# Optimization experiments

Hardware: AMD Instinct MI355X
Metric: run time of the kernel (lower is better)

## Reference

```python
import jax, jax.numpy as jnp
import numpy as np

EPS = 1e-5  # torch LayerNorm default eps

def _mish(x):
    return x * jnp.tanh(jax.nn.softplus(x))

def _ln(x, g, b):
    mu = jnp.mean(x, axis=-1, keepdims=True)
    var = jnp.mean(jnp.square(x - mu), axis=-1, keepdims=True)
    return (x - mu) * jax.lax.rsqrt(var + EPS) * g + b

def setup_inputs() -> dict:
    key = jax.random.key(0)
    ks = jax.random.split(key, 10)
    B, D, O1, O2, O3 = 65536, 784, 512, 264, 128
    def lin(k, fan_in, shape):
        bound = 1.0 / np.sqrt(fan_in)
        return jax.random.uniform(k, shape, jnp.float32, -bound, bound)
    return {
        "x":  jax.random.uniform(ks[0], (B, D), jnp.float32),
        "W1": lin(ks[1], D,  (O1, D)),   # enFC1, bias=False
        "g1": jnp.ones((O1,), jnp.float32), "b1": jnp.zeros((O1,), jnp.float32),
        "W2": lin(ks[2], O1, (O2, O1)),  # enFC2, bias=False
        "g2": jnp.ones((O2,), jnp.float32), "b2": jnp.zeros((O2,), jnp.float32),
        "W3": lin(ks[3], O2, (O3, O2)),  # enFC3 with bias
        "b3": lin(ks[4], O2, (O3,)),
        "gh": jnp.ones((O3,), jnp.float32), "bh": jnp.zeros((O3,), jnp.float32),
        "D1": lin(ks[5], O3, (O2, O3)),  # deFC1, bias=False
        "g3": jnp.ones((O2,), jnp.float32), "b3n": jnp.zeros((O2,), jnp.float32),
        "D2": lin(ks[6], O2, (O1, O2)),  # deFC2, bias=False
        "g4": jnp.ones((O1,), jnp.float32), "b4": jnp.zeros((O1,), jnp.float32),
        "D3": lin(ks[7], O1, (D, O1)),   # deFC3 with bias
        "bo": lin(ks[8], O1, (D,)),
    }

def reference(x, W1, g1, b1, W2, g2, b2, W3, b3, gh, bh,
              D1, g3, b3n, D2, g4, b4, D3, bo):
    h = _mish(_ln(x @ W1.T, g1, b1))
    h = _mish(_ln(h @ W2.T, g2, b2))
    x_latent = _mish(_ln(h @ W3.T + b3, gh, bh))
    h = _mish(_ln(x_latent @ D1.T, g3, b3n))
    h = _mish(_ln(h @ D2.T, g4, b4))
    out = jax.nn.sigmoid(h @ D3.T + bo)
    return out, jnp.sum(jnp.abs(x_latent))
```

## Files before the change

### kernel.cpp

```cpp
#include <hip/hip_runtime.h>


typedef short bf16x8 __attribute__((ext_vector_type(8)));
typedef float f32x4  __attribute__((ext_vector_type(4)));

#define B_ROWS 65536
#define EPS_LN 1e-5f

static __device__ __forceinline__ unsigned short f2bf(float f) {
    union { float f; unsigned u; } v; v.f = f;
    unsigned r = v.u + 0x7FFFu + ((v.u >> 16) & 1u);
    return (unsigned short)(r >> 16);
}

static __device__ __forceinline__ float mish_f(float x) {
    if (x > 15.f) return x;
    float u = __expf(x);
    float p = __fmaf_rn(u, u, 2.f * u);
    return x * (p / (p + 2.f));
}

static __device__ __forceinline__ void glds16(const void* g, void* l) {
    typedef __attribute__((address_space(3))) unsigned lds_u32;
    typedef __attribute__((address_space(1))) const unsigned glb_u32;
    lds_u32* lp = (lds_u32*)l;
    unsigned lofs = __builtin_amdgcn_readfirstlane((unsigned)(unsigned long long)lp);
    lp = (lds_u32*)(unsigned long long)lofs;
    __builtin_amdgcn_global_load_lds((glb_u32*)g, lp, 16, 0, 0);
}

struct CvtArgs {
    const float* src[6];
    unsigned short* dst[6];
    int O[6], K[6], KP[6];
    int base[7];
};

__global__ void wpad_kernel(CvtArgs a) {
    int b = blockIdx.x;
    int seg = 0;
    while (b >= a.base[seg + 1]) ++seg;
    int r = b - a.base[seg];
    int O = a.O[seg], K = a.K[seg], KP = a.KP[seg];
    const float* s = a.src[seg];
    unsigned short* d = a.dst[seg];
    for (int c = threadIdx.x; c < KP; c += 256) {
        unsigned short v = 0;
        if (r < O && c < K) v = f2bf(s[(size_t)r * K + c]);
        d[(size_t)r * KP + c] = v;
    }
}

template<int KP, int ASTR, int KREAL, int OP, int OREAL, int OSTRIDE, int NKT,
         bool SRCF32, bool HASBIAS, bool ABS, bool LN>
__global__ __launch_bounds__(1024, 4)
void layer3(const void* __restrict__ Asrc,
            const unsigned short* __restrict__ Wp,
            const float* __restrict__ gam,
            const float* __restrict__ bet,
            const float* __restrict__ bias,
            void* __restrict__ Aout,
            float* __restrict__ partials,
            int cbase)
{
    constexpr int NT     = OP / 128;
    constexpr int NCH_W  = OP / 16;
    constexpr int ABYTES = 128 * 64;
    constexpr int WBYTES = OP * 64;

    __shared__ __align__(16) char smem[2 * ABYTES + 2 * WBYTES];

    const int tid  = threadIdx.x;
    const int wave = tid >> 6, lane = tid & 63;
    const int wr = wave >> 3, wc = wave & 7;
    const int lg = lane >> 4, lc = lane & 15;
    const int row0 = blockIdx.x * 128;

    size_t goW[2];
    int    loW[2];
#pragma unroll
    for (int i = 0; i < 2; ++i) {
        int j = wave + 16 * i;
        if (j < NCH_W) {
            int q = j * 64 + lane;
            int r = q >> 2;
            int sg = (q & 3) ^ ((r >> 1) & 3);
            goW[i] = ((size_t)(cbase + r) * KP + sg * 8) * 2;
            loW[i] = 2 * ABYTES + j * 1024;
        } else { goW[i] = 0; loW[i] = 0; }
    }
    size_t goA = 0; int loA = 0;
    if constexpr (!SRCF32) {
        if (wave < 8) {
            int q = wave * 64 + lane;
            int r = q >> 2;
            int sg = (q & 3) ^ ((r >> 1) & 3);
            goA = ((size_t)(row0 + r) * ASTR + sg * 8) * 2;
            loA = wave * 1024;
        }
    }

    const char* Wg = (const char*)Wp;
    const char* Ag = (const char*)Asrc;

    float4 rA0 = make_float4(0,0,0,0), rA1 = make_float4(0,0,0,0);
    const int ar = tid >> 2, as = tid & 3;
    const float* axp = (const float*)Asrc + (size_t)(row0 + ar) * ASTR + as * 8;
    const int aswz = ar * 64 + ((as ^ ((ar >> 1) & 3)) << 4);

    auto loadA1 = [&](int t) {
        int c0 = t * 32 + as * 8;
        rA0 = (c0     < KREAL) ? *(const float4*)(axp + t * 32)     : make_float4(0,0,0,0);
        rA1 = (c0 + 4 < KREAL) ? *(const float4*)(axp + t * 32 + 4) : make_float4(0,0,0,0);
    };
    auto pubA = [&](int bsel) {
        union { unsigned short us[8]; uint4 v; } u;
        u.us[0] = f2bf(rA0.x); u.us[1] = f2bf(rA0.y);
        u.us[2] = f2bf(rA0.z); u.us[3] = f2bf(rA0.w);
        u.us[4] = f2bf(rA1.x); u.us[5] = f2bf(rA1.y);
        u.us[6] = f2bf(rA1.z); u.us[7] = f2bf(rA1.w);
        *(uint4*)(smem + bsel * ABYTES + aswz) = u.v;
    };
    auto stageW = [&](int t, int bsel) {
#pragma unroll
        for (int i = 0; i < 2; ++i)
            if (wave + 16 * i < NCH_W)
                glds16(Wg + goW[i] + (size_t)t * 64, smem + loW[i] + bsel * WBYTES);
        if constexpr (!SRCF32) {
            if (wave < 8)
                glds16(Ag + goA + (size_t)t * 64, smem + loA + bsel * ABYTES);
        }
    };

    stageW(0, 0);
    if constexpr (SRCF32) {
        if (tid < 512) { loadA1(0); pubA(0); if (NKT > 1) loadA1(1); }
    }
    __syncthreads();

    f32x4 acc[4][NT];
#pragma unroll
    for (int a = 0; a < 4; ++a)
#pragma unroll
        for (int c = 0; c < NT; ++c) acc[a][c] = (f32x4){0.f, 0.f, 0.f, 0.f};

    const int fswz = ((lg ^ ((lc >> 1) & 3)) << 4);

    for (int t = 0; t < NKT; ++t) {
        const int bsel = t & 1;
        if (t + 1 < NKT) stageW(t + 1, bsel ^ 1);

        const char* Ab = smem + bsel * ABYTES + (wr * 64 + lc) * 64 + fswz;
        const char* Bb = smem + 2 * ABYTES + bsel * WBYTES + (wc * NT * 16 + lc) * 64 + fswz;
        bf16x8 afr[4], bfr[NT];
#pragma unroll
        for (int a = 0; a < 4; ++a) afr[a] = *(const bf16x8*)(Ab + a * 1024);
#pragma unroll
        for (int c = 0; c < NT; ++c) bfr[c] = *(const bf16x8*)(Bb + c * 1024);

        if constexpr (SRCF32) {
            if (tid < 512) {
                if (t + 1 < NKT) pubA(bsel ^ 1);
                if (t + 2 < NKT) loadA1(t + 2);
            }
        }
        __builtin_amdgcn_sched_barrier(0);
#pragma unroll
        for (int c = 0; c < NT; ++c)
#pragma unroll
            for (int a = 0; a < 4; ++a)
                acc[a][c] = __builtin_amdgcn_mfma_f32_16x16x32_bf16(afr[a], bfr[c], acc[a][c], 0, 0, 0);
        __syncthreads();
    }

    if constexpr (LN) {
        if constexpr (HASBIAS) {
#pragma unroll
            for (int c = 0; c < NT; ++c) {
                int col = wc * NT * 16 + c * 16 + lc;
                float bv = (col < OREAL) ? bias[col] : 0.f;
#pragma unroll
                for (int a = 0; a < 4; ++a)
#pragma unroll
                    for (int r = 0; r < 4; ++r) acc[a][c][r] += bv;
            }
        }
        float ps1[4][4], ps2[4][4];
#pragma unroll
        for (int a = 0; a < 4; ++a)
#pragma unroll
            for (int r = 0; r < 4; ++r) { ps1[a][r] = 0.f; ps2[a][r] = 0.f; }
#pragma unroll
        for (int a = 0; a < 4; ++a)
#pragma unroll
            for (int c = 0; c < NT; ++c)
#pragma unroll
                for (int r = 0; r < 4; ++r) {
                    float v = acc[a][c][r];
                    ps1[a][r] += v;
                    ps2[a][r] = __fmaf_rn(v, v, ps2[a][r]);
                }
#pragma unroll
        for (int m = 1; m < 16; m <<= 1)
#pragma unroll
            for (int a = 0; a < 4; ++a)
#pragma unroll
                for (int r = 0; r < 4; ++r) {
                    ps1[a][r] += __shfl_xor(ps1[a][r], m);
                    ps2[a][r] += __shfl_xor(ps2[a][r], m);
                }

        float* lnP  = (float*)smem;
        float* lnMR = (float*)smem + 2048;
        float* wsumP= (float*)smem + 2304;

        if (lc == 0) {
#pragma unroll
            for (int a = 0; a < 4; ++a)
#pragma unroll
                for (int r = 0; r < 4; ++r) {
                    int row = wr * 64 + a * 16 + lg * 4 + r;
                    lnP[row * 8 + wc]        = ps1[a][r];
                    lnP[1024 + row * 8 + wc] = ps2[a][r];
                }
        }
        __syncthreads();
        if (tid < 128) {
            float s1 = 0.f, s2 = 0.f;
#pragma unroll
            for (int w = 0; w < 8; ++w) { s1 += lnP[tid * 8 + w]; s2 += lnP[1024 + tid * 8 + w]; }
            float mu = s1 * (1.f / OREAL);
            float var = fmaxf(s2 * (1.f / OREAL) - mu * mu, 0.f);
            lnMR[tid]       = mu;
            lnMR[128 + tid] = rsqrtf(var + EPS_LN);
        }
        __syncthreads();

        float gcol[NT], bcol[NT];
#pragma unroll
        for (int c = 0; c < NT; ++c) {
            int col = wc * NT * 16 + c * 16 + lc;
            gcol[c] = (col < OREAL) ? gam[col] : 0.f;
            bcol[c] = (col < OREAL) ? bet[col] : 0.f;
        }

        float asum = 0.f;
        unsigned short* outp = (unsigned short*)Aout;
#pragma unroll
        for (int a = 0; a < 4; ++a)
#pragma unroll
            for (int r = 0; r < 4; ++r) {
                int rl = wr * 64 + a * 16 + lg * 4 + r;
                float mu = lnMR[rl], rs = lnMR[128 + rl];
                size_t rowoff = (size_t)(row0 + rl) * OSTRIDE;
#pragma unroll
                for (int c = 0; c < NT; ++c) {
                    int col = wc * NT * 16 + c * 16 + lc;
                    if (col < OSTRIDE) {
                        unsigned short outv = 0;
                        if (col < OREAL) {
                            float v = (acc[a][c][r] - mu) * rs * gcol[c] + bcol[c];
                            float mz = mish_f(v);
                            if (ABS) asum += fabsf(mz);
                            outv = f2bf(mz);
                        }
                        outp[rowoff + col] = outv;
                    }
                }
            }

        if constexpr (ABS) {
#pragma unroll
            for (int m = 1; m < 64; m <<= 1) asum += __shfl_xor(asum, m);
            if (lane == 0) wsumP[wave] = asum;
            __syncthreads();
            if (tid == 0) {
                float s = 0.f;
                for (int w = 0; w < 16; ++w) s += wsumP[w];
                partials[blockIdx.x] = s;
            }
        }
    } else {
        float* outp = (float*)Aout;
#pragma unroll
        for (int c = 0; c < NT; ++c) {
            int col = cbase + wc * NT * 16 + c * 16 + lc;
            bool ok = col < OREAL;
            float bv = ok ? bias[col] : 0.f;
#pragma unroll
            for (int a = 0; a < 4; ++a)
#pragma unroll
                for (int r = 0; r < 4; ++r) {
                    if (ok) {
                        int rl = wr * 64 + a * 16 + lg * 4 + r;
                        float v = acc[a][c][r] + bv;
                        outp[(size_t)(row0 + rl) * OSTRIDE + col] = 1.f / (1.f + __expf(-v));
                    }
                }
        }
    }
}

__global__ void reduce_abs(const float* __restrict__ partials, float* __restrict__ out) {
    __shared__ float sm[256];
    float s = 0.f;
    for (int i = threadIdx.x; i < 512; i += 256) s += partials[i];
    sm[threadIdx.x] = s;
    __syncthreads();
    for (int step = 128; step > 0; step >>= 1) {
        if (threadIdx.x < step) sm[threadIdx.x] += sm[threadIdx.x + step];
        __syncthreads();
    }
    if (threadIdx.x == 0) out[0] = sm[0];
}

extern "C" void kernel_launch(void* const* d_in, const int* in_sizes, int n_in,
                              void* d_out, int out_size, void* d_ws, size_t ws_size,
                              hipStream_t stream)
{
    const float* x   = (const float*)d_in[0];
    const float* W1  = (const float*)d_in[1];
    const float* g1  = (const float*)d_in[2];
    const float* b1  = (const float*)d_in[3];
    const float* W2  = (const float*)d_in[4];
    const float* g2  = (const float*)d_in[5];
    const float* b2  = (const float*)d_in[6];
    const float* W3  = (const float*)d_in[7];
    const float* b3  = (const float*)d_in[8];
    const float* gh  = (const float*)d_in[9];
    const float* bh  = (const float*)d_in[10];
    const float* D1  = (const float*)d_in[11];
    const float* g3  = (const float*)d_in[12];
    const float* b3n = (const float*)d_in[13];
    const float* D2  = (const float*)d_in[14];
    const float* g4  = (const float*)d_in[15];
    const float* b4  = (const float*)d_in[16];
    const float* D3  = (const float*)d_in[17];
    const float* bo  = (const float*)d_in[18];

    char* ws = (char*)d_ws;
    size_t off = 0;
    auto alloc = [&](size_t bytes) -> char* {
        char* p = ws + off;
        off += (bytes + 255) & ~(size_t)255;
        return p;
    };
    unsigned short* W1p = (unsigned short*)alloc((size_t)512 * 800 * 2);
    unsigned short* W2p = (unsigned short*)alloc((size_t)384 * 512 * 2);
    unsigned short* W3p = (unsigned short*)alloc((size_t)128 * 288 * 2);
    unsigned short* D1p = (unsigned short*)alloc((size_t)384 * 128 * 2);
    unsigned short* D2p = (unsigned short*)alloc((size_t)512 * 288 * 2);
    unsigned short* D3p = (unsigned short*)alloc((size_t)896 * 512 * 2);
    unsigned short* actP = (unsigned short*)alloc((size_t)B_ROWS * 512 * 2);
    unsigned short* actQ = (unsigned short*)alloc((size_t)B_ROWS * 288 * 2);
    unsigned short* actL = (unsigned short*)alloc((size_t)B_ROWS * 128 * 2);
    float* partials = (float*)alloc(512 * 4);

    CvtArgs ca;
    ca.src[0] = W1; ca.dst[0] = W1p; ca.O[0] = 512; ca.K[0] = 784; ca.KP[0] = 800;
    ca.src[1] = W2; ca.dst[1] = W2p; ca.O[1] = 264; ca.K[1] = 512; ca.KP[1] = 512;
    ca.src[2] = W3; ca.dst[2] = W3p; ca.O[2] = 128; ca.K[2] = 264; ca.KP[2] = 288;
    ca.src[3] = D1; ca.dst[3] = D1p; ca.O[3] = 264; ca.K[3] = 128; ca.KP[3] = 128;
    ca.src[4] = D2; ca.dst[4] = D2p; ca.O[4] = 512; ca.K[4] = 264; ca.KP[4] = 288;
    ca.src[5] = D3; ca.dst[5] = D3p; ca.O[5] = 784; ca.K[5] = 512; ca.KP[5] = 512;
    ca.base[0] = 0;    ca.base[1] = 512;  ca.base[2] = 896;
    ca.base[3] = 1024; ca.base[4] = 1408; ca.base[5] = 1920; ca.base[6] = 2816;
    wpad_kernel<<<2816, 256, 0, stream>>>(ca);

    const int NB = B_ROWS / 128;

    layer3<800, 784, 784, 512, 512, 512, 25, true,  false, false, true>
        <<<NB, 1024, 0, stream>>>(x, W1p, g1, b1, nullptr, actP, nullptr, 0);
    layer3<512, 512, 512, 384, 264, 288, 16, false, false, false, true>
        <<<NB, 1024, 0, stream>>>(actP, W2p, g2, b2, nullptr, actQ, nullptr, 0);
    layer3<288, 288, 288, 128, 128, 128, 9,  false, true,  true,  true>
        <<<NB, 1024, 0, stream>>>(actQ, W3p, gh, bh, b3, actL, partials, 0);
    layer3<128, 128, 128, 384, 264, 288, 4,  false, false, false, true>
        <<<NB, 1024, 0, stream>>>(actL, D1p, g3, b3n, nullptr, actQ, nullptr, 0);
    layer3<288, 288, 288, 512, 512, 512, 9,  false, false, false, true>
        <<<NB, 1024, 0, stream>>>(actQ, D2p, g4, b4, nullptr, actP, nullptr, 0);
    layer3<512, 512, 512, 512, 784, 784, 16, false, true,  false, false>
        <<<NB, 1024, 0, stream>>>(actP, D3p, nullptr, nullptr, bo, d_out, nullptr, 0);
    layer3<512, 512, 512, 384, 784, 784, 16, false, true,  false, false>
        <<<NB, 1024, 0, stream>>>(actP, D3p, nullptr, nullptr, bo, d_out, nullptr, 512);

    reduce_abs<<<1, 256, 0, stream>>>(partials, (float*)d_out + (size_t)B_ROWS * 784);
}
```

Baseline: 479.5 us.

## Triple-buffer K-loop staging with explicit vmcnt waits and raw barriers

Converts the GEMM K-loop from double to triple buffering in LDS, prefetching two tiles ahead instead of one. Weight and activation chunks are unified into one staging table. Full __syncthreads is replaced by per-wave s_waitcnt vmcnt counts plus a raw s_barrier, so waves only wait for the oldest outstanding tile. This aims to hide global-to-LDS latency better, at the cost of more LDS per block (possible occupancy loss) and fragile hand-counted waitcnt logic.

```diff
diff --git a/kernel.cpp b/kernel.cpp
--- a/kernel.cpp
+++ b/kernel.cpp
@@ -27,6 +27,24 @@
     unsigned lofs = __builtin_amdgcn_readfirstlane((unsigned)(unsigned long long)lp);
     lp = (lds_u32*)(unsigned long long)lofs;
     __builtin_amdgcn_global_load_lds((glb_u32*)g, lp, 16, 0, 0);
+}
+
+template<int N> __device__ __forceinline__ void vwait() {
+    if constexpr      (N <= 0) asm volatile("s_waitcnt vmcnt(0)" ::: "memory");
+    else if constexpr (N == 1) asm volatile("s_waitcnt vmcnt(1)" ::: "memory");
+    else if constexpr (N == 2) asm volatile("s_waitcnt vmcnt(2)" ::: "memory");
+    else if constexpr (N == 3) asm volatile("s_waitcnt vmcnt(3)" ::: "memory");
+    else if constexpr (N == 4) asm volatile("s_waitcnt vmcnt(4)" ::: "memory");
+    else if constexpr (N == 5) asm volatile("s_waitcnt vmcnt(5)" ::: "memory");
+    else if constexpr (N == 6) asm volatile("s_waitcnt vmcnt(6)" ::: "memory");
+    else if constexpr (N == 8) asm volatile("s_waitcnt vmcnt(8)" ::: "memory");
+    else                       asm volatile("s_waitcnt vmcnt(63)" ::: "memory");
+}
+
+static __device__ __forceinline__ void barrier_raw() {
+    asm volatile("" ::: "memory");
+    __builtin_amdgcn_s_barrier();
+    asm volatile("" ::: "memory");
 }
 
 struct CvtArgs {
@@ -54,7 +72,7 @@
 template<int KP, int ASTR, int KREAL, int OP, int OREAL, int OSTRIDE, int NKT,
          bool SRCF32, bool HASBIAS, bool ABS, bool LN>
 __global__ __launch_bounds__(1024, 4)
-void layer3(const void* __restrict__ Asrc,
+void layer4(const void* __restrict__ Asrc,
             const unsigned short* __restrict__ Wp,
             const float* __restrict__ gam,
             const float* __restrict__ bet,
@@ -63,12 +81,17 @@
             float* __restrict__ partials,
             int cbase)
 {
-    constexpr int NT     = OP / 128;
-    constexpr int NCH_W  = OP / 16;
-    constexpr int ABYTES = 128 * 64;
-    constexpr int WBYTES = OP * 64;
-
-    __shared__ __align__(16) char smem[2 * ABYTES + 2 * WBYTES];
+    constexpr int NT      = OP / 128;
+    constexpr int NCH_W   = OP / 16;
+    constexpr int NCH_TOT = NCH_W + (SRCF32 ? 0 : 8);
+    constexpr int MAXC    = (NCH_TOT + 15) / 16;
+    constexpr int ABYTES  = 128 * 64;
+    constexpr int WBYTES  = OP * 64;
+    constexpr int WBASE   = 3 * ABYTES;
+    constexpr int LVL     = (NCH_TOT - 1 - 0) / 16 + 1;
+    constexpr int LVH     = (NCH_TOT - 1 - 8) / 16 + 1;
+
+    __shared__ __align__(16) char smem[WBASE + 3 * WBYTES];
 
     const int tid  = threadIdx.x;
     const int wave = tid >> 6, lane = tid & 63;
@@ -76,67 +99,63 @@
     const int lg = lane >> 4, lc = lane & 15;
     const int row0 = blockIdx.x * 128;
 
-    size_t goW[2];
-    int    loW[2];
-#pragma unroll
-    for (int i = 0; i < 2; ++i) {
-        int j = wave + 16 * i;
-        if (j < NCH_W) {
-            int q = j * 64 + lane;
-            int r = q >> 2;
-            int sg = (q & 3) ^ ((r >> 1) & 3);
-            goW[i] = ((size_t)(cbase + r) * KP + sg * 8) * 2;
-            loW[i] = 2 * ABYTES + j * 1024;
-        } else { goW[i] = 0; loW[i] = 0; }
-    }
-    size_t goA = 0; int loA = 0;
-    if constexpr (!SRCF32) {
-        if (wave < 8) {
-            int q = wave * 64 + lane;
-            int r = q >> 2;
-            int sg = (q & 3) ^ ((r >> 1) & 3);
-            goA = ((size_t)(row0 + r) * ASTR + sg * 8) * 2;
-            loA = wave * 1024;
-        }
-    }
-
-    const char* Wg = (const char*)Wp;
-    const char* Ag = (const char*)Asrc;
-
-    float4 rA0 = make_float4(0,0,0,0), rA1 = make_float4(0,0,0,0);
+    const char* gp[MAXC];
+    int lo[MAXC], lstr[MAXC];
+#pragma unroll
+    for (int i = 0; i < MAXC; ++i) {
+        int c = wave + 16 * i;
+        gp[i] = nullptr; lo[i] = 0; lstr[i] = 0;
+        if (c < NCH_W) {
+            int row = c * 16 + (lane >> 2);
+            int sg = (lane & 3) ^ ((row >> 1) & 3);
+            gp[i] = (const char*)Wp + ((size_t)(cbase + row) * KP + sg * 8) * 2;
+            lo[i] = WBASE + c * 1024; lstr[i] = WBYTES;
+        } else if (c < NCH_TOT) {
+            int ca = c - NCH_W;
+            int row = ca * 16 + (lane >> 2);
+            int sg = (lane & 3) ^ ((row >> 1) & 3);
+            gp[i] = (const char*)Asrc + ((size_t)(row0 + row) * ASTR + sg * 8) * 2;
+            lo[i] = ca * 1024; lstr[i] = ABYTES;
+        }
+    }
+    auto stage = [&](int t, int b) {
+#pragma unroll
+        for (int i = 0; i < MAXC; ++i) {
+            int c = wave + 16 * i;
+            if (c < NCH_TOT)
+                glds16(gp[i] + (size_t)t * 64, smem + lo[i] + b * lstr[i]);
+        }
+    };
+
     const int ar = tid >> 2, as = tid & 3;
     const float* axp = (const float*)Asrc + (size_t)(row0 + ar) * ASTR + as * 8;
     const int aswz = ar * 64 + ((as ^ ((ar >> 1) & 3)) << 4);
+    float4 rA0 = make_float4(0,0,0,0), rA1 = make_float4(0,0,0,0);
 
     auto loadA1 = [&](int t) {
         int c0 = t * 32 + as * 8;
         rA0 = (c0     < KREAL) ? *(const float4*)(axp + t * 32)     : make_float4(0,0,0,0);
         rA1 = (c0 + 4 < KREAL) ? *(const float4*)(axp + t * 32 + 4) : make_float4(0,0,0,0);
     };
-    auto pubA = [&](int bsel) {
+    auto pubA = [&](int b) {
         union { unsigned short us[8]; uint4 v; } u;
         u.us[0] = f2bf(rA0.x); u.us[1] = f2bf(rA0.y);
         u.us[2] = f2bf(rA0.z); u.us[3] = f2bf(rA0.w);
         u.us[4] = f2bf(rA1.x); u.us[5] = f2bf(rA1.y);
         u.us[6] = f2bf(rA1.z); u.us[7] = f2bf(rA1.w);
-        *(uint4*)(smem + bsel * ABYTES + aswz) = u.v;
+        *(uint4*)(smem + b * ABYTES + aswz) = u.v;
     };
-    auto stageW = [&](int t, int bsel) {
-#pragma unroll
-        for (int i = 0; i < 2; ++i)
-            if (wave + 16 * i < NCH_W)
-                glds16(Wg + goW[i] + (size_t)t * 64, smem + loW[i] + bsel * WBYTES);
-        if constexpr (!SRCF32) {
-            if (wave < 8)
-                glds16(Ag + goA + (size_t)t * 64, smem + loA + bsel * ABYTES);
-        }
-    };
-
-    stageW(0, 0);
+
+    stage(0, 0);
+    if constexpr (SRCF32) { if (tid < 512) loadA1(0); }
+    stage(1, 1);
     if constexpr (SRCF32) {
-        if (tid < 512) { loadA1(0); pubA(0); if (NKT > 1) loadA1(1); }
-    }
-    __syncthreads();
+        if (tid < 512) {
+            pubA(0);
+            loadA1(1);
+            asm volatile("s_waitcnt lgkmcnt(0)" ::: "memory");
+        }
+    }
 
     f32x4 acc[4][NT];
 #pragma unroll
@@ -146,12 +165,35 @@
 
     const int fswz = ((lg ^ ((lc >> 1) & 3)) << 4);
 
+    int bc = 0, bp = 1, bs = 2;
     for (int t = 0; t < NKT; ++t) {
-        const int bsel = t & 1;
-        if (t + 1 < NKT) stageW(t + 1, bsel ^ 1);
-
-        const char* Ab = smem + bsel * ABYTES + (wr * 64 + lc) * 64 + fswz;
-        const char* Bb = smem + 2 * ABYTES + bsel * WBYTES + (wc * NT * 16 + lc) * 64 + fswz;
+        if (t + 2 < NKT) stage(t + 2, bs);
+
+        if constexpr (SRCF32) {
+            if (wave >= 8) {
+                if      (t + 2 < NKT) vwait<2 * LVL>();
+                else if (t + 1 < NKT) vwait<LVL>();
+                else                  vwait<0>();
+            }
+        } else if constexpr (LVL == LVH) {
+            if      (t + 2 < NKT) vwait<2 * LVL>();
+            else if (t + 1 < NKT) vwait<LVL>();
+            else                  vwait<0>();
+        } else {
+            if (wave < 8) {
+                if      (t + 2 < NKT) vwait<2 * LVL>();
+                else if (t + 1 < NKT) vwait<LVL>();
+                else                  vwait<0>();
+            } else {
+                if      (t + 2 < NKT) vwait<2 * LVH>();
+                else if (t + 1 < NKT) vwait<LVH>();
+                else                  vwait<0>();
+            }
+        }
+        barrier_raw();
+
+        const char* Ab = smem + bc * ABYTES + (wr * 64 + lc) * 64 + fswz;
+        const char* Bb = smem + WBASE + bc * WBYTES + (wc * NT * 16 + lc) * 64 + fswz;
         bf16x8 afr[4], bfr[NT];
 #pragma unroll
         for (int a = 0; a < 4; ++a) afr[a] = *(const bf16x8*)(Ab + a * 1024);
@@ -160,17 +202,19 @@
 
         if constexpr (SRCF32) {
             if (tid < 512) {
-                if (t + 1 < NKT) pubA(bsel ^ 1);
+                if (t + 1 < NKT) pubA(bp);
                 if (t + 2 < NKT) loadA1(t + 2);
             }
         }
-        __builtin_amdgcn_sched_barrier(0);
 #pragma unroll
         for (int c = 0; c < NT; ++c)
 #pragma unroll
             for (int a = 0; a < 4; ++a)
                 acc[a][c] = __builtin_amdgcn_mfma_f32_16x16x32_bf16(afr[a], bfr[c], acc[a][c], 0, 0, 0);
-        __syncthreads();
+
+        if constexpr (SRCF32) asm volatile("s_waitcnt lgkmcnt(0)" ::: "memory");
+        barrier_raw();
+        int tmp = bc; bc = bp; bp = bs; bs = tmp;
     }
 
     if constexpr (LN) {
@@ -210,9 +254,9 @@
                     ps2[a][r] += __shfl_xor(ps2[a][r], m);
                 }
 
-        float* lnP  = (float*)smem;
-        float* lnMR = (float*)smem + 2048;
-        float* wsumP= (float*)smem + 2304;
+        float* lnP   = (float*)smem;
+        float* lnMR  = (float*)smem + 2048;
+        float* wsumP = (float*)smem + 2304;
 
         if (lc == 0) {
 #pragma unroll
@@ -369,19 +413,19 @@
 
     const int NB = B_ROWS / 128;
 
-    layer3<800, 784, 784, 512, 512, 512, 25, true,  false, false, true>
+    layer4<800, 784, 784, 512, 512, 512, 25, true,  false, false, true>
         <<<NB, 1024, 0, stream>>>(x, W1p, g1, b1, nullptr, actP, nullptr, 0);
-    layer3<512, 512, 512, 384, 264, 288, 16, false, false, false, true>
+    layer4<512, 512, 512, 384, 264, 288, 16, false, false, false, true>
         <<<NB, 1024, 0, stream>>>(actP, W2p, g2, b2, nullptr, actQ, nullptr, 0);
-    layer3<288, 288, 288, 128, 128, 128, 9,  false, true,  true,  true>
+    layer4<288, 288, 288, 128, 128, 128, 9,  false, true,  true,  true>
         <<<NB, 1024, 0, stream>>>(actQ, W3p, gh, bh, b3, actL, partials, 0);
-    layer3<128, 128, 128, 384, 264, 288, 4,  false, false, false, true>
+    layer4<128, 128, 128, 384, 264, 288, 4,  false, false, false, true>
         <<<NB, 1024, 0, stream>>>(actL, D1p, g3, b3n, nullptr, actQ, nullptr, 0);
-    layer3<288, 288, 288, 512, 512, 512, 9,  false, false, false, true>
+    layer4<288, 288, 288, 512, 512, 512, 9,  false, false, false, true>
         <<<NB, 1024, 0, stream>>>(actQ, D2p, g4, b4, nullptr, actP, nullptr, 0);
-    layer3<512, 512, 512, 512, 784, 784, 16, false, true,  false, false>
+    layer4<512, 512, 512, 512, 784, 784, 16, false, true,  false, false>
         <<<NB, 1024, 0, stream>>>(actP, D3p, nullptr, nullptr, bo, d_out, nullptr, 0);
-    layer3<512, 512, 512, 384, 784, 784, 16, false, true,  false, false>
+    layer4<512, 512, 512, 384, 784, 784, 16, false, true,  false, false>
         <<<NB, 1024, 0, stream>>>(actP, D3p, nullptr, nullptr, bo, d_out, nullptr, 512);
 
     reduce_abs<<<1, 256, 0, stream>>>(partials, (float*)d_out + (size_t)B_ROWS * 784);
```

Result: no change. 479.4 us (-0.0%).

## Shrink row tiles to 64 and parameterize wave layout per layer

Applied to the files above, without the earlier changes.

Replaces the fixed 128-row, 16-wave kernel with a templated version that uses 64-row tiles and a configurable wave count and wave-row split. Each layer gets its own block size (256 or 512 threads). The last layer becomes one 2D-grid launch over four 224-column slices instead of two launches of 512 and 384 columns. Smaller blocks raise block count and occupancy and cut LN-reduction overhead, but each weight tile is now reused across fewer rows, which raises weight traffic per output. The sched_barrier is also removed.

```diff
diff --git a/kernel.cpp b/kernel.cpp
--- a/kernel.cpp
+++ b/kernel.cpp
@@ -52,95 +52,90 @@
 }
 
 template<int KP, int ASTR, int KREAL, int OP, int OREAL, int OSTRIDE, int NKT,
-         bool SRCF32, bool HASBIAS, bool ABS, bool LN>
-__global__ __launch_bounds__(1024, 4)
-void layer3(const void* __restrict__ Asrc,
+         int NW, int WR, bool SRCF32, bool HASBIAS, bool ABS, bool LN>
+__global__ __launch_bounds__(NW * 64, 4)
+void layer5(const void* __restrict__ Asrc,
             const unsigned short* __restrict__ Wp,
             const float* __restrict__ gam,
             const float* __restrict__ bet,
             const float* __restrict__ bias,
             void* __restrict__ Aout,
-            float* __restrict__ partials,
-            int cbase)
+            float* __restrict__ partials)
 {
-    constexpr int NT     = OP / 128;
-    constexpr int NCH_W  = OP / 16;
-    constexpr int ABYTES = 128 * 64;
-    constexpr int WBYTES = OP * 64;
-
-    __shared__ __align__(16) char smem[2 * ABYTES + 2 * WBYTES];
+    constexpr int WC    = NW / WR;
+    constexpr int NT    = OP / (WC * 16);
+    constexpr int AR    = 4 / WR;
+    constexpr int WROWS = 16 * AR;
+    constexpr int NCH_W = OP / 16;
+    constexpr int NCH   = NCH_W + (SRCF32 ? 0 : 4);
+    constexpr int MAXC  = (NCH + NW - 1) / NW;
+    constexpr int ABY   = 4096;
+    constexpr int WBY   = OP * 64;
+
+    __shared__ __align__(16) char smem[2 * ABY + 2 * WBY];
 
     const int tid  = threadIdx.x;
     const int wave = tid >> 6, lane = tid & 63;
-    const int wr = wave >> 3, wc = wave & 7;
+    const int wrI = wave / WC, wcI = wave % WC;
     const int lg = lane >> 4, lc = lane & 15;
-    const int row0 = blockIdx.x * 128;
-
-    size_t goW[2];
-    int    loW[2];
-#pragma unroll
-    for (int i = 0; i < 2; ++i) {
-        int j = wave + 16 * i;
-        if (j < NCH_W) {
-            int q = j * 64 + lane;
-            int r = q >> 2;
-            int sg = (q & 3) ^ ((r >> 1) & 3);
-            goW[i] = ((size_t)(cbase + r) * KP + sg * 8) * 2;
-            loW[i] = 2 * ABYTES + j * 1024;
-        } else { goW[i] = 0; loW[i] = 0; }
-    }
-    size_t goA = 0; int loA = 0;
-    if constexpr (!SRCF32) {
-        if (wave < 8) {
-            int q = wave * 64 + lane;
-            int r = q >> 2;
-            int sg = (q & 3) ^ ((r >> 1) & 3);
-            goA = ((size_t)(row0 + r) * ASTR + sg * 8) * 2;
-            loA = wave * 1024;
-        }
-    }
-
-    const char* Wg = (const char*)Wp;
-    const char* Ag = (const char*)Asrc;
-
-    float4 rA0 = make_float4(0,0,0,0), rA1 = make_float4(0,0,0,0);
+    const int row0  = blockIdx.x * 64;
+    const int cbase = blockIdx.y * OP;
+
+    const char* gp[MAXC];
+#pragma unroll
+    for (int i = 0; i < MAXC; ++i) {
+        int c = wave + NW * i;
+        gp[i] = nullptr;
+        if (c < NCH_W) {
+            int row = c * 16 + (lane >> 2);
+            int sg = (lane & 3) ^ ((row >> 1) & 3);
+            gp[i] = (const char*)Wp + ((size_t)(cbase + row) * KP + sg * 8) * 2;
+        } else if (c < NCH) {
+            int row = (c - NCH_W) * 16 + (lane >> 2);
+            int sg = (lane & 3) ^ ((row >> 1) & 3);
+            gp[i] = (const char*)Asrc + ((size_t)(row0 + row) * ASTR + sg * 8) * 2;
+        }
+    }
+    auto stage = [&](int t, int b) {
+#pragma unroll
+        for (int i = 0; i < MAXC; ++i) {
+            int c = wave + NW * i;
+            if (c < NCH) {
+                int off = (c < NCH_W) ? (2 * ABY + b * WBY + c * 1024)
+                                      : (b * ABY + (c - NCH_W) * 1024);
+                glds16(gp[i] + (size_t)t * 64, smem + off);
+            }
+        }
+    };
+
     const int ar = tid >> 2, as = tid & 3;
     const float* axp = (const float*)Asrc + (size_t)(row0 + ar) * ASTR + as * 8;
     const int aswz = ar * 64 + ((as ^ ((ar >> 1) & 3)) << 4);
+    float4 rA0 = make_float4(0,0,0,0), rA1 = make_float4(0,0,0,0);
 
     auto loadA1 = [&](int t) {
         int c0 = t * 32 + as * 8;
         rA0 = (c0     < KREAL) ? *(const float4*)(axp + t * 32)     : make_float4(0,0,0,0);
         rA1 = (c0 + 4 < KREAL) ? *(const float4*)(axp + t * 32 + 4) : make_float4(0,0,0,0);
     };
-    auto pubA = [&](int bsel) {
+    auto pubA = [&](int b) {
         union { unsigned short us[8]; uint4 v; } u;
         u.us[0] = f2bf(rA0.x); u.us[1] = f2bf(rA0.y);
         u.us[2] = f2bf(rA0.z); u.us[3] = f2bf(rA0.w);
         u.us[4] = f2bf(rA1.x); u.us[5] = f2bf(rA1.y);
         u.us[6] = f2bf(rA1.z); u.us[7] = f2bf(rA1.w);
-        *(uint4*)(smem + bsel * ABYTES + aswz) = u.v;
+        *(uint4*)(smem + b * ABY + aswz) = u.v;
     };
-    auto stageW = [&](int t, int bsel) {
-#pragma unroll
-        for (int i = 0; i < 2; ++i)
-            if (wave + 16 * i < NCH_W)
-                glds16(Wg + goW[i] + (size_t)t * 64, smem + loW[i] + bsel * WBYTES);
-        if constexpr (!SRCF32) {
-            if (wave < 8)
-                glds16(Ag + goA + (size_t)t * 64, smem + loA + bsel * ABYTES);
-        }
-    };
-
-    stageW(0, 0);
+
+    stage(0, 0);
     if constexpr (SRCF32) {
-        if (tid < 512) { loadA1(0); pubA(0); if (NKT > 1) loadA1(1); }
+        if (tid < 256) { loadA1(0); pubA(0); if (NKT > 1) loadA1(1); }
     }
     __syncthreads();
 
-    f32x4 acc[4][NT];
-#pragma unroll
-    for (int a = 0; a < 4; ++a)
+    f32x4 acc[AR][NT];
+#pragma unroll
+    for (int a = 0; a < AR; ++a)
 #pragma unroll
         for (int c = 0; c < NT; ++c) acc[a][c] = (f32x4){0.f, 0.f, 0.f, 0.f};
 
@@ -148,27 +143,26 @@
 
     for (int t = 0; t < NKT; ++t) {
         const int bsel = t & 1;
-        if (t + 1 < NKT) stageW(t + 1, bsel ^ 1);
-
-        const char* Ab = smem + bsel * ABYTES + (wr * 64 + lc) * 64 + fswz;
-        const char* Bb = smem + 2 * ABYTES + bsel * WBYTES + (wc * NT * 16 + lc) * 64 + fswz;
-        bf16x8 afr[4], bfr[NT];
-#pragma unroll
-        for (int a = 0; a < 4; ++a) afr[a] = *(const bf16x8*)(Ab + a * 1024);
+        if (t + 1 < NKT) stage(t + 1, bsel ^ 1);
+
+        const char* Ab = smem + bsel * ABY + (wrI * WROWS + lc) * 64 + fswz;
+        const char* Bb = smem + 2 * ABY + bsel * WBY + (wcI * NT * 16 + lc) * 64 + fswz;
+        bf16x8 afr[AR], bfr[NT];
+#pragma unroll
+        for (int a = 0; a < AR; ++a) afr[a] = *(const bf16x8*)(Ab + a * 1024);
 #pragma unroll
         for (int c = 0; c < NT; ++c) bfr[c] = *(const bf16x8*)(Bb + c * 1024);
 
         if constexpr (SRCF32) {
-            if (tid < 512) {
+            if (tid < 256) {
                 if (t + 1 < NKT) pubA(bsel ^ 1);
                 if (t + 2 < NKT) loadA1(t + 2);
             }
         }
-        __builtin_amdgcn_sched_barrier(0);
 #pragma unroll
         for (int c = 0; c < NT; ++c)
 #pragma unroll
-            for (int a = 0; a < 4; ++a)
+            for (int a = 0; a < AR; ++a)
                 acc[a][c] = __builtin_amdgcn_mfma_f32_16x16x32_bf16(afr[a], bfr[c], acc[a][c], 0, 0, 0);
         __syncthreads();
     }
@@ -177,21 +171,21 @@
         if constexpr (HASBIAS) {
 #pragma unroll
             for (int c = 0; c < NT; ++c) {
-                int col = wc * NT * 16 + c * 16 + lc;
+                int col = wcI * NT * 16 + c * 16 + lc;
                 float bv = (col < OREAL) ? bias[col] : 0.f;
 #pragma unroll
-                for (int a = 0; a < 4; ++a)
+                for (int a = 0; a < AR; ++a)
 #pragma unroll
                     for (int r = 0; r < 4; ++r) acc[a][c][r] += bv;
             }
         }
-        float ps1[4][4], ps2[4][4];
-#pragma unroll
-        for (int a = 0; a < 4; ++a)
+        float ps1[AR][4], ps2[AR][4];
+#pragma unroll
+        for (int a = 0; a < AR; ++a)
 #pragma unroll
             for (int r = 0; r < 4; ++r) { ps1[a][r] = 0.f; ps2[a][r] = 0.f; }
 #pragma unroll
-        for (int a = 0; a < 4; ++a)
+        for (int a = 0; a < AR; ++a)
 #pragma unroll
             for (int c = 0; c < NT; ++c)
 #pragma unroll
@@ -203,43 +197,43 @@
 #pragma unroll
         for (int m = 1; m < 16; m <<= 1)
 #pragma unroll
-            for (int a = 0; a < 4; ++a)
+            for (int a = 0; a < AR; ++a)
 #pragma unroll
                 for (int r = 0; r < 4; ++r) {
                     ps1[a][r] += __shfl_xor(ps1[a][r], m);
                     ps2[a][r] += __shfl_xor(ps2[a][r], m);
                 }
 
-        float* lnP  = (float*)smem;
-        float* lnMR = (float*)smem + 2048;
-        float* wsumP= (float*)smem + 2304;
+        float* lnP   = (float*)smem;
+        float* lnMR  = (float*)smem + 1024;
+        float* wsumP = (float*)smem + 1152;
 
         if (lc == 0) {
 #pragma unroll
-            for (int a = 0; a < 4; ++a)
+            for (int a = 0; a < AR; ++a)
 #pragma unroll
                 for (int r = 0; r < 4; ++r) {
-                    int row = wr * 64 + a * 16 + lg * 4 + r;
-                    lnP[row * 8 + wc]        = ps1[a][r];
-                    lnP[1024 + row * 8 + wc] = ps2[a][r];
+                    int row = a * 16 + lg * 4 + r;
+                    lnP[row * 8 + wcI]       = ps1[a][r];
+                    lnP[512 + row * 8 + wcI] = ps2[a][r];
                 }
         }
         __syncthreads();
-        if (tid < 128) {
+        if (tid < 64) {
             float s1 = 0.f, s2 = 0.f;
 #pragma unroll
-            for (int w = 0; w < 8; ++w) { s1 += lnP[tid * 8 + w]; s2 += lnP[1024 + tid * 8 + w]; }
+            for (int w = 0; w < WC; ++w) { s1 += lnP[tid * 8 + w]; s2 += lnP[512 + tid * 8 + w]; }
             float mu = s1 * (1.f / OREAL);
             float var = fmaxf(s2 * (1.f / OREAL) - mu * mu, 0.f);
-            lnMR[tid]       = mu;
-            lnMR[128 + tid] = rsqrtf(var + EPS_LN);
+            lnMR[tid]      = mu;
+            lnMR[64 + tid] = rsqrtf(var + EPS_LN);
         }
         __syncthreads();
 
         float gcol[NT], bcol[NT];
 #pragma unroll
         for (int c = 0; c < NT; ++c) {
-            int col = wc * NT * 16 + c * 16 + lc;
+            int col = wcI * NT * 16 + c * 16 + lc;
             gcol[c] = (col < OREAL) ? gam[col] : 0.f;
             bcol[c] = (col < OREAL) ? bet[col] : 0.f;
         }
@@ -247,15 +241,15 @@
         float asum = 0.f;
         unsigned short* outp = (unsigned short*)Aout;
 #pragma unroll
-        for (int a = 0; a < 4; ++a)
+        for (int a = 0; a < AR; ++a)
 #pragma unroll
             for (int r = 0; r < 4; ++r) {
-                int rl = wr * 64 + a * 16 + lg * 4 + r;
-                float mu = lnMR[rl], rs = lnMR[128 + rl];
+                int rl = a * 16 + lg * 4 + r;
+                float mu = lnMR[rl], rs = lnMR[64 + rl];
                 size_t rowoff = (size_t)(row0 + rl) * OSTRIDE;
 #pragma unroll
                 for (int c = 0; c < NT; ++c) {
-                    int col = wc * NT * 16 + c * 16 + lc;
+                    int col = wcI * NT * 16 + c * 16 + lc;
                     if (col < OSTRIDE) {
                         unsigned short outv = 0;
                         if (col < OREAL) {
@@ -276,7 +270,7 @@
             __syncthreads();
             if (tid == 0) {
                 float s = 0.f;
-                for (int w = 0; w < 16; ++w) s += wsumP[w];
+                for (int w = 0; w < NW; ++w) s += wsumP[w];
                 partials[blockIdx.x] = s;
             }
         }
@@ -284,15 +278,15 @@
         float* outp = (float*)Aout;
 #pragma unroll
         for (int c = 0; c < NT; ++c) {
-            int col = cbase + wc * NT * 16 + c * 16 + lc;
+            int col = cbase + wcI * NT * 16 + c * 16 + lc;
             bool ok = col < OREAL;
             float bv = ok ? bias[col] : 0.f;
 #pragma unroll
-            for (int a = 0; a < 4; ++a)
+            for (int a = 0; a < AR; ++a)
 #pragma unroll
                 for (int r = 0; r < 4; ++r) {
                     if (ok) {
-                        int rl = wr * 64 + a * 16 + lg * 4 + r;
+                        int rl = wrI * WROWS + a * 16 + lg * 4 + r;
                         float v = acc[a][c][r] + bv;
                         outp[(size_t)(row0 + rl) * OSTRIDE + col] = 1.f / (1.f + __expf(-v));
                     }
@@ -304,7 +298,7 @@
 __global__ void reduce_abs(const float* __restrict__ partials, float* __restrict__ out) {
     __shared__ float sm[256];
     float s = 0.f;
-    for (int i = threadIdx.x; i < 512; i += 256) s += partials[i];
+    for (int i = threadIdx.x; i < 1024; i += 256) s += partials[i];
     sm[threadIdx.x] = s;
     __syncthreads();
     for (int step = 128; step > 0; step >>= 1) {
@@ -354,7 +348,7 @@
     unsigned short* actP = (unsigned short*)alloc((size_t)B_ROWS * 512 * 2);
     unsigned short* actQ = (unsigned short*)alloc((size_t)B_ROWS * 288 * 2);
     unsigned short* actL = (unsigned short*)alloc((size_t)B_ROWS * 128 * 2);
-    float* partials = (float*)alloc(512 * 4);
+    float* partials = (float*)alloc(1024 * 4);
 
     CvtArgs ca;
     ca.src[0] = W1; ca.dst[0] = W1p; ca.O[0] = 512; ca.K[0] = 784; ca.KP[0] = 800;
@@ -367,22 +361,21 @@
     ca.base[3] = 1024; ca.base[4] = 1408; ca.base[5] = 1920; ca.base[6] = 2816;
     wpad_kernel<<<2816, 256, 0, stream>>>(ca);
 
-    const int NB = B_ROWS / 128;
-
-    layer3<800, 784, 784, 512, 512, 512, 25, true,  false, false, true>
-        <<<NB, 1024, 0, stream>>>(x, W1p, g1, b1, nullptr, actP, nullptr, 0);
-    layer3<512, 512, 512, 384, 264, 288, 16, false, false, false, true>
-        <<<NB, 1024, 0, stream>>>(actP, W2p, g2, b2, nullptr, actQ, nullptr, 0);
-    layer3<288, 288, 288, 128, 128, 128, 9,  false, true,  true,  true>
-        <<<NB, 1024, 0, stream>>>(actQ, W3p, gh, bh, b3, actL, partials, 0);
-    layer3<128, 128, 128, 384, 264, 288, 4,  false, false, false, true>
-        <<<NB, 1024, 0, stream>>>(actL, D1p, g3, b3n, nullptr, actQ, nullptr, 0);
-    layer3<288, 288, 288, 512, 512, 512, 9,  false, false, false, true>
-        <<<NB, 1024, 0, stream>>>(actQ, D2p, g4, b4, nullptr, actP, nullptr, 0);
-    layer3<512, 512, 512, 512, 784, 784, 16, false, true,  false, false>
-        <<<NB, 1024, 0, stream>>>(actP, D3p, nullptr, nullptr, bo, d_out, nullptr, 0);
-    layer3<512, 512, 512, 384, 784, 784, 16, false, true,  false, false>
-        <<<NB, 1024, 0, stream>>>(actP, D3p, nullptr, nullptr, bo, d_out, nullptr, 512);
+    const int NB = B_ROWS / 64;
+
+    layer5<800, 784, 784, 512, 512, 512, 25, 8, 1, true,  false, false, true>
+        <<<NB, 512, 0, stream>>>(x, W1p, g1, b1, nullptr, actP, nullptr);
+    layer5<512, 512, 512, 384, 264, 288, 16, 8, 1, false, false, false, true>
+        <<<NB, 512, 0, stream>>>(actP, W2p, g2, b2, nullptr, actQ, nullptr);
+    layer5<288, 288, 288, 128, 128, 128, 9,  4, 1, false, true,  true,  true>
+        <<<NB, 256, 0, stream>>>(actQ, W3p, gh, bh, b3, actL, partials);
+    layer5<128, 128, 128, 384, 264, 288, 4,  8, 1, false, false, false, true>
+        <<<NB, 512, 0, stream>>>(actL, D1p, g3, b3n, nullptr, actQ, nullptr);
+    layer5<288, 288, 288, 512, 512, 512, 9,  8, 1, false, false, false, true>
+        <<<NB, 512, 0, stream>>>(actQ, D2p, g4, b4, nullptr, actP, nullptr);
+    dim3 g6(NB, 4);
+    layer5<512, 512, 512, 224, 784, 784, 16, 4, 2, false, true,  false, false>
+        <<<g6, 256, 0, stream>>>(actP, D3p, nullptr, nullptr, bo, d_out, nullptr);
 
     reduce_abs<<<1, 256, 0, stream>>>(partials, (float*)d_out + (size_t)B_ROWS * 784);
 }
```

New measurement: 485.6 us. No clear change (+1.3%).
